# Performance work log

Hardware: AMD Instinct MI355X
Metric: run time of the kernel (lower is better)

Reference implementation:

```python
import jax, jax.numpy as jnp
import numpy as np
from jax import lax


def setup_inputs() -> dict:
    key = jax.random.key(0)
    ks = jax.random.split(key, 6)
    T, B, I, H = 512, 64, 1024, 1024
    f16 = jnp.float16
    # scale weights down so fp16 activations stay in range
    return {
        "x": jax.random.normal(ks[0], (T, B, I), dtype=f16),
        "h0": jax.random.normal(ks[1], (1, B, H), dtype=f16),
        "w_ih": (jax.random.normal(ks[2], (3 * H, I), dtype=f16) * f16(0.02)),
        "w_hh": (jax.random.normal(ks[3], (3 * H, H), dtype=f16) * f16(0.02)),
        "b_ih": jax.random.normal(ks[4], (3 * H,), dtype=f16),
        "b_hh": jax.random.normal(ks[5], (3 * H,), dtype=f16),
    }


def reference(x, h0, w_ih, w_hh, b_ih, b_hh):
    # Single-layer GRU forward, PyTorch gate order (r, z, n).
    # fp16 storage, fp32 accumulation, hidden state re-quantized to fp16
    # each timestep (matches the fused CUDA kernel's shared-memory half buffer).
    f32 = jnp.float32
    H = h0.shape[-1]
    wih = w_ih.astype(f32)   # (3H, I)
    whh = w_hh.astype(f32)   # (3H, H)
    bih = b_ih.astype(f32)
    bhh = b_hh.astype(f32)

    # Precompute input-projection for all timesteps: (T, B, 3H)
    gi = jnp.einsum('tbi,gi->tbg', x.astype(f32), wih) + bih

    def step(h_prev16, gi_t):
        h_prev = h_prev16.astype(f32)                       # (B, H)
        gh = h_prev @ whh.T + bhh                           # (B, 3H)
        ir, iz, inn = gi_t[:, :H], gi_t[:, H:2 * H], gi_t[:, 2 * H:]
        hr, hz, hn = gh[:, :H], gh[:, H:2 * H], gh[:, 2 * H:]
        r = jax.nn.sigmoid(ir + hr)
        z = jax.nn.sigmoid(iz + hz)
        n = jnp.tanh(inn + r * hn)
        h_new = ((1.0 - z) * n + z * h_prev).astype(jnp.float16)
        return h_new, h_new

    _, y = lax.scan(step, h0[0], gi)                        # y: (T, B, H) fp16
    return y
```

## Files before the change

### kernel.cpp

```cpp
#include <hip/hip_runtime.h>
#include <hip/hip_bf16.h>
#include <hip/hip_fp16.h>


typedef __attribute__((ext_vector_type(8))) _Float16 f16x8;
typedef __attribute__((ext_vector_type(4))) float f32x4;
typedef __attribute__((ext_vector_type(8))) float f32x8;

#define MFMA(a, b, c) __builtin_amdgcn_mfma_f32_16x16x32_f16((a), (b), (c), 0, 0, 0)

#define T_T 512
#define T_B 64
#define T_K 1024
#define T_N3 3072

__device__ float          g_gi[(size_t)T_T * T_B * T_N3];
__device__ unsigned short g_hbf[(size_t)T_T * T_B * T_K];
__device__ unsigned       g_flags[64 * 32];
__device__ unsigned short g_xh[(size_t)T_T * T_B * T_K];
__device__ unsigned short g_wh[(size_t)T_N3 * T_K];

static __device__ __forceinline__ f16x8 cvt8(f32x8 v) {
    f16x8 r;
    #pragma unroll
    for (int i = 0; i < 8; ++i) r[i] = (_Float16)v[i];
    return r;
}
static __device__ __forceinline__ float sigmoidf_(float x) {
    return 1.0f / (1.0f + __expf(-x));
}
static __device__ __forceinline__ float tanhf_(float x) {
    return 2.0f / (1.0f + __expf(-2.0f * x)) - 1.0f;
}

__global__ __launch_bounds__(256) void reset_flags_k() {
    for (int i = threadIdx.x; i < 64 * 32; i += 256) g_flags[i] = 0;
}

__global__ __launch_bounds__(256) void cvt_k(
    const float* __restrict__ X,
    const float* __restrict__ W)
{
    const size_t NX = (size_t)T_T * T_B * T_K / 8;
    const size_t NW = (size_t)T_N3 * T_K / 8;
    size_t i0 = (size_t)blockIdx.x * 256 + threadIdx.x;
    size_t stride = (size_t)gridDim.x * 256;
    for (size_t i = i0; i < NX; i += stride)
        ((f16x8*)g_xh)[i] = cvt8(((const f32x8*)X)[i]);
    for (size_t i = i0; i < NW; i += stride)
        ((f16x8*)g_wh)[i] = cvt8(((const f32x8*)W)[i]);
}

__global__ __launch_bounds__(256) void gi_gemm(
    const float* __restrict__ bih)
{
    __shared__ __align__(16) unsigned short lA[128 * 32];
    __shared__ __align__(16) unsigned short lB[128 * 32];
    const int tid  = threadIdx.x;
    const int lane = tid & 63;
    const int wid  = tid >> 6;
    const int swz = (blockIdx.x & 7) * 768 + (blockIdx.x >> 3);
    const int m0 = (swz / 24) * 128;
    const int n0 = (swz % 24) * 128;
    const int wm = wid >> 1, wn = wid & 1;

    const int srow = tid >> 2;
    const int skc  = tid & 3;

    f32x4 acc[4][4] = {};

    for (int k0 = 0; k0 < T_K; k0 += 32) {
        #pragma unroll
        for (int i = 0; i < 2; ++i) {
            const unsigned short* ga =
                g_xh + (size_t)(m0 + i * 64 + srow) * T_K + k0 + skc * 8;
            const unsigned short* gb =
                g_wh + (size_t)(n0 + i * 64 + srow) * T_K + k0 + skc * 8;
            char* la = (char*)lA + i * 4096 + wid * 1024;
            char* lb = (char*)lB + i * 4096 + wid * 1024;
            __builtin_amdgcn_global_load_lds(
                (const __attribute__((address_space(1))) unsigned int*)ga,
                (__attribute__((address_space(3))) unsigned int*)la, 16, 0, 0);
            __builtin_amdgcn_global_load_lds(
                (const __attribute__((address_space(1))) unsigned int*)gb,
                (__attribute__((address_space(3))) unsigned int*)lb, 16, 0, 0);
        }
        __syncthreads();

        f16x8 a[4], b[4];
        #pragma unroll
        for (int mt = 0; mt < 4; ++mt) {
            int row = 64 * wm + 16 * mt + (lane & 15);
            a[mt] = *(const f16x8*)((const char*)lA + row * 64 + (lane >> 4) * 16);
        }
        #pragma unroll
        for (int nt = 0; nt < 4; ++nt) {
            int row = 64 * wn + 16 * nt + (lane & 15);
            b[nt] = *(const f16x8*)((const char*)lB + row * 64 + (lane >> 4) * 16);
        }
        #pragma unroll
        for (int mt = 0; mt < 4; ++mt)
            #pragma unroll
            for (int nt = 0; nt < 4; ++nt)
                acc[mt][nt] = MFMA(a[mt], b[nt], acc[mt][nt]);
        __syncthreads();
    }

    #pragma unroll
    for (int mt = 0; mt < 4; ++mt) {
        int rbase = m0 + 64 * wm + 16 * mt + (lane >> 4) * 4;
        #pragma unroll
        for (int nt = 0; nt < 4; ++nt) {
            int col = n0 + 64 * wn + 16 * nt + (lane & 15);
            float bv = bih[col];
            #pragma unroll
            for (int j = 0; j < 4; ++j)
                g_gi[(size_t)(rbase + j) * T_N3 + col] = acc[mt][nt][j] + bv;
        }
    }
}

__global__ __launch_bounds__(256, 1) void gru_scan(
    const float* __restrict__ Whh,
    const float* __restrict__ Bhh,
    const float* __restrict__ H0,
    float* Y)
{
    __shared__ unsigned short Wl[48 * 1024];
    const int tid  = threadIdx.x;
    const int lane = tid & 63;
    const int w    = tid >> 6;
    const int c0   = blockIdx.x * 16;

    for (int idx = tid; idx < 48 * 128; idx += 256) {
        int row = idx >> 7;
        int kc  = idx & 127;
        int gate = row >> 4, cc = row & 15;
        f32x8 v = *(const f32x8*)(Whh + (size_t)(gate * 1024 + c0 + cc) * T_K + kc * 8);
        *(f16x8*)((char*)Wl + kc * 768 + row * 16) = cvt8(v);
    }
    const int colL = c0 + (lane & 15);
    const float br = Bhh[colL];
    const float bz = Bhh[1024 + colL];
    const float bn = Bhh[2048 + colL];
    __syncthreads();

    const char* bbase = (const char*)Wl + (lane >> 4) * 768 + (lane & 15) * 16;

    float pr[4], pz[4], pn[4];
    #pragma unroll
    for (int j = 0; j < 4; ++j) {
        int row = 16 * w + (lane >> 4) * 4 + j;
        pr[j] = g_gi[(size_t)row * T_N3 + colL];
        pz[j] = g_gi[(size_t)row * T_N3 + 1024 + colL];
        pn[j] = g_gi[(size_t)row * T_N3 + 2048 + colL];
    }

    float hreg[4];

    for (int t = 0; t < T_T; ++t) {
        f32x4 ar = {0.f, 0.f, 0.f, 0.f}, az = ar, an = ar;

        if (t == 0) {
            const float* abase =
                H0 + (size_t)(16 * w + (lane & 15)) * T_K + (lane >> 4) * 8;
            #pragma unroll 4
            for (int kk = 0; kk < 32; ++kk) {
                f16x8 af = cvt8(*(const f32x8*)(abase + kk * 32));
                const char* bb = bbase + kk * 3072;
                ar = MFMA(af, *(const f16x8*)(bb),       ar);
                az = MFMA(af, *(const f16x8*)(bb + 256), az);
                an = MFMA(af, *(const f16x8*)(bb + 512), an);
            }
        } else {
            const unsigned short* abase = g_hbf + (size_t)(t - 1) * (T_B * T_K)
                + (size_t)(16 * w + (lane & 15)) * T_K + (lane >> 4) * 8;
            f16x8 af[32];
            #pragma unroll
            for (int kk = 0; kk < 32; ++kk)
                af[kk] = *(const f16x8*)(abase + kk * 32);
            asm volatile("" ::: "memory");
            #pragma unroll
            for (int kk = 0; kk < 32; ++kk) {
                const char* bb = bbase + kk * 3072;
                ar = MFMA(af[kk], *(const f16x8*)(bb),       ar);
                az = MFMA(af[kk], *(const f16x8*)(bb + 256), az);
                an = MFMA(af[kk], *(const f16x8*)(bb + 512), an);
            }
        }

        #pragma unroll
        for (int j = 0; j < 4; ++j) {
            int row = 16 * w + (lane >> 4) * 4 + j;
            size_t off = (size_t)row * T_K + colL;
            float hp = (t == 0) ? H0[off] : hreg[j];
            float r = sigmoidf_(pr[j] + ar[j] + br);
            float z = sigmoidf_(pz[j] + az[j] + bz);
            float n = tanhf_(pn[j] + r * (an[j] + bn));
            float h = (1.0f - z) * n + z * hp;
            __half h16 = __float2half(h);
            float  hq  = __half2float(h16);
            hreg[j] = hq;
            Y[(size_t)t * (T_B * T_K) + off] = hq;

            unsigned v16 = (unsigned)__half_as_ushort(h16);
            unsigned up  = __shfl_xor(v16, 1);
            if (!(lane & 1)) {
                unsigned packed = v16 | (up << 16);
                unsigned* dst = (unsigned*)(g_hbf + (size_t)t * (T_B * T_K) + off);
                __hip_atomic_store(dst, packed, __ATOMIC_RELAXED,
                                   __HIP_MEMORY_SCOPE_AGENT);
            }
        }

        if (t + 1 < T_T) {
            asm volatile("s_waitcnt vmcnt(0)" ::: "memory");
            __syncthreads();
            if (tid == 0)
                __hip_atomic_store(&g_flags[blockIdx.x * 32], (unsigned)(t + 1),
                                   __ATOMIC_RELAXED, __HIP_MEMORY_SCOPE_AGENT);

            const float* g = g_gi + (size_t)(t + 1) * T_B * T_N3;
            #pragma unroll
            for (int j = 0; j < 4; ++j) {
                int row = 16 * w + (lane >> 4) * 4 + j;
                pr[j] = g[(size_t)row * T_N3 + colL];
                pz[j] = g[(size_t)row * T_N3 + 1024 + colL];
                pn[j] = g[(size_t)row * T_N3 + 2048 + colL];
            }

            if (w == 0) {
                unsigned tgt = (unsigned)(t + 1);
                for (;;) {
                    unsigned v = __hip_atomic_load(&g_flags[lane * 32],
                                                   __ATOMIC_RELAXED,
                                                   __HIP_MEMORY_SCOPE_AGENT);
                    if (__all((int)(v >= tgt))) break;
                    __builtin_amdgcn_s_sleep(1);
                }
            }
            asm volatile("" ::: "memory");
            __syncthreads();
        }
    }
}

extern "C" void kernel_launch(void* const* d_in, const int* in_sizes, int n_in,
                              void* d_out, int out_size, void* d_ws, size_t ws_size,
                              hipStream_t stream)
{
    const float* X   = (const float*)d_in[0];
    const float* H0  = (const float*)d_in[1];
    const float* Wih = (const float*)d_in[2];
    const float* Whh = (const float*)d_in[3];
    const float* Bih = (const float*)d_in[4];
    const float* Bhh = (const float*)d_in[5];
    float* Y = (float*)d_out;
    (void)d_ws; (void)ws_size; (void)in_sizes; (void)n_in; (void)out_size;

    reset_flags_k<<<dim3(1), dim3(256), 0, stream>>>();

    cvt_k<<<dim3(2048), dim3(256), 0, stream>>>(X, Wih);

    gi_gemm<<<dim3(256 * 24), dim3(256), 0, stream>>>(Bih);

    gru_scan<<<dim3(64), dim3(256), 0, stream>>>(Whh, Bhh, H0, Y);
}
```

Baseline: 4.366 ms.

## Double-buffer gi GEMM LDS tiles and defer Y stores off the scan critical path

The input-projection GEMM now uses two LDS buffers, so the next K-slice is loaded while MFMAs run on the current one, and one barrier per iteration is dropped. In the recurrent scan, each step's output store to Y moves to the start of the next step. That keeps those stores out of the vmcnt(0) wait before the flag publish, which is the latency-critical inter-block sync. The changes cost double the LDS in the GEMM and add one extra store loop after the scan loop.

New measurement: 4.403 ms. No clear change (+0.9%).

```diff
diff --git a/kernel.cpp b/kernel.cpp
--- a/kernel.cpp
+++ b/kernel.cpp
@@ -54,8 +54,8 @@
 __global__ __launch_bounds__(256) void gi_gemm(
     const float* __restrict__ bih)
 {
-    __shared__ __align__(16) unsigned short lA[128 * 32];
-    __shared__ __align__(16) unsigned short lB[128 * 32];
+    __shared__ __align__(16) unsigned short lA[2][128 * 32];
+    __shared__ __align__(16) unsigned short lB[2][128 * 32];
     const int tid  = threadIdx.x;
     const int lane = tid & 63;
     const int wid  = tid >> 6;
@@ -67,17 +67,15 @@
     const int srow = tid >> 2;
     const int skc  = tid & 3;
 
-    f32x4 acc[4][4] = {};
-
-    for (int k0 = 0; k0 < T_K; k0 += 32) {
+    auto stage = [&](int buf, int k0) {
         #pragma unroll
         for (int i = 0; i < 2; ++i) {
             const unsigned short* ga =
                 g_xh + (size_t)(m0 + i * 64 + srow) * T_K + k0 + skc * 8;
             const unsigned short* gb =
                 g_wh + (size_t)(n0 + i * 64 + srow) * T_K + k0 + skc * 8;
-            char* la = (char*)lA + i * 4096 + wid * 1024;
-            char* lb = (char*)lB + i * 4096 + wid * 1024;
+            char* la = (char*)lA + buf * 8192 + i * 4096 + wid * 1024;
+            char* lb = (char*)lB + buf * 8192 + i * 4096 + wid * 1024;
             __builtin_amdgcn_global_load_lds(
                 (const __attribute__((address_space(1))) unsigned int*)ga,
                 (__attribute__((address_space(3))) unsigned int*)la, 16, 0, 0);
@@ -85,24 +83,36 @@
                 (const __attribute__((address_space(1))) unsigned int*)gb,
                 (__attribute__((address_space(3))) unsigned int*)lb, 16, 0, 0);
         }
-        __syncthreads();
+    };
+
+    f32x4 acc[4][4] = {};
+
+    stage(0, 0);
+    __syncthreads();
+
+    for (int it = 0; it < 32; ++it) {
+        const int cur = it & 1;
+        if (it < 31) stage(cur ^ 1, (it + 1) * 32);
 
         f16x8 a[4], b[4];
         #pragma unroll
         for (int mt = 0; mt < 4; ++mt) {
             int row = 64 * wm + 16 * mt + (lane & 15);
-            a[mt] = *(const f16x8*)((const char*)lA + row * 64 + (lane >> 4) * 16);
+            a[mt] = *(const f16x8*)((const char*)lA + cur * 8192
+                                    + row * 64 + (lane >> 4) * 16);
         }
         #pragma unroll
         for (int nt = 0; nt < 4; ++nt) {
             int row = 64 * wn + 16 * nt + (lane & 15);
-            b[nt] = *(const f16x8*)((const char*)lB + row * 64 + (lane >> 4) * 16);
+            b[nt] = *(const f16x8*)((const char*)lB + cur * 8192
+                                    + row * 64 + (lane >> 4) * 16);
         }
         #pragma unroll
         for (int mt = 0; mt < 4; ++mt)
             #pragma unroll
             for (int nt = 0; nt < 4; ++nt)
                 acc[mt][nt] = MFMA(a[mt], b[nt], acc[mt][nt]);
+
         __syncthreads();
     }
 
@@ -159,6 +169,14 @@
     float hreg[4];
 
     for (int t = 0; t < T_T; ++t) {
+        if (t > 0) {
+            #pragma unroll
+            for (int j = 0; j < 4; ++j) {
+                int row = 16 * w + (lane >> 4) * 4 + j;
+                Y[(size_t)(t - 1) * (T_B * T_K) + (size_t)row * T_K + colL] = hreg[j];
+            }
+        }
+
         f32x4 ar = {0.f, 0.f, 0.f, 0.f}, az = ar, an = ar;
 
         if (t == 0) {
@@ -201,7 +219,6 @@
             __half h16 = __float2half(h);
             float  hq  = __half2float(h16);
             hreg[j] = hq;
-            Y[(size_t)t * (T_B * T_K) + off] = hq;
 
             unsigned v16 = (unsigned)__half_as_ushort(h16);
             unsigned up  = __shfl_xor(v16, 1);
@@ -243,6 +260,12 @@
             __syncthreads();
         }
     }
+
+    #pragma unroll
+    for (int j = 0; j < 4; ++j) {
+        int row = 16 * w + (lane >> 4) * 4 + j;
+        Y[(size_t)(T_T - 1) * (T_B * T_K) + (size_t)row * T_K + colL] = hreg[j];
+    }
 }
 
 extern "C" void kernel_launch(void* const* d_in, const int* in_sizes, int n_in,
```
